# Optimization experiments

Measured on AMD Instinct MI355X. Metric: run time of the kernel, lower is better.

Reference implementation:

```python
import jax, jax.numpy as jnp
import numpy as np

CHUNK = 64  # mamba chunk size


def _ssd_chunk_scan(x, dt, A, Bs, Cs, R):
    """Exact chunked selective scan (mamba_chunk_scan_combined math, no D skip).
    x: [B,L,H,P] (H=K*R heads), dt: [B,L,H] (already softplus'd),
    A: [H], Bs/Cs: [B,L,K,N] groups (head h uses group h//R).
    Returns y: [B,L,H,P]."""
    Bsz, L, Hh, P = x.shape
    K, N = Bs.shape[2], Bs.shape[3]
    Nc = L // CHUNK
    # broadcast groups -> heads (head k*R+r uses group k)
    Bh = jnp.repeat(Bs, R, axis=2)  # [B,L,H,N]
    Ch = jnp.repeat(Cs, R, axis=2)
    xc = x.reshape(Bsz, Nc, CHUNK, Hh, P)
    dtc = dt.reshape(Bsz, Nc, CHUNK, Hh)
    Bc = Bh.reshape(Bsz, Nc, CHUNK, Hh, N)
    Cc = Ch.reshape(Bsz, Nc, CHUNK, Hh, N)
    dA = jnp.transpose(dtc, (0, 1, 3, 2)) * A[None, None, :, None]  # [B,Nc,H,Q]
    Acum = jnp.cumsum(dA, axis=-1)
    # intra-chunk decay matrix Lmat[i,j] = exp(sum_{j<s<=i} dA_s), lower-tri
    diff = Acum[..., :, None] - Acum[..., None, :]  # [B,Nc,H,Q,Q]
    tri = jnp.tril(jnp.ones((CHUNK, CHUNK), bool))
    Lmat = jnp.where(tri, jnp.exp(diff), 0.0)
    xdt = xc * dtc[..., None]  # dt enters as dt_j * B_j * x_j
    Y_diag = jnp.einsum('bcqhn,bcshn,bchqs,bcshp->bcqhp', Cc, Bc, Lmat, xdt)
    # chunk end states
    decay_last = jnp.exp(Acum[..., -1:] - Acum)  # [B,Nc,H,Q]
    states = jnp.einsum('bcqhn,bchq,bcqhp->bchpn', Bc, decay_last, xdt)
    chunk_decay = jnp.exp(Acum[..., -1])  # [B,Nc,H]
    def step(S, inp):
        cd, st = inp
        return cd[..., None, None] * S + st, S  # emit state BEFORE this chunk
    S0 = jnp.zeros((Bsz, Hh, P, N), x.dtype)
    _, prev = jax.lax.scan(step, S0, (jnp.moveaxis(chunk_decay, 1, 0), jnp.moveaxis(states, 1, 0)))
    prev = jnp.moveaxis(prev, 0, 1)  # [B,Nc,H,P,N]
    Y_off = jnp.einsum('bcqhn,bchpn,bchq->bcqhp', Cc, prev, jnp.exp(Acum))
    return (Y_diag + Y_off).reshape(Bsz, L, Hh, P)


def _forward(x, in_proj_w, conv_w, conv_b, x_proj_w, A_logs, Ds, dt_bias,
             out_norm_g, out_norm_b, out_proj_w):
    B, H, W, Dm = x.shape
    K, R = A_logs.shape
    P = Ds.shape[2]               # headdim
    d_inner = x_proj_w.shape[2]
    N = (x_proj_w.shape[1] - R) // 2
    L = H * W
    # in_proj + gate split
    xz = jnp.einsum('bhwc,dc->bhwd', x, in_proj_w)
    xi, z = jnp.split(xz, 2, axis=-1)
    z = jax.nn.gelu(z, approximate=False)
    # depthwise 3x3 conv (torch weight [d_inner,1,3,3] -> HWIO [3,3,1,d_inner])
    kern = jnp.transpose(conv_w, (2, 3, 1, 0))
    xi = jax.lax.conv_general_dilated(xi, kern, (1, 1), 'SAME',
            dimension_numbers=('NHWC', 'HWIO', 'NHWC'),
            feature_group_count=d_inner) + conv_b
    xi = jax.nn.gelu(xi, approximate=False)
    # cross2d scan: row-major, col-major, and their reverses
    x0 = xi.reshape(B, L, d_inner)
    x1 = jnp.transpose(xi, (0, 2, 1, 3)).reshape(B, L, d_inner)
    xs = jnp.stack([x0, x1, x0[:, ::-1], x1[:, ::-1]], axis=2)  # [B,L,K,d_inner]
    x_dbl = jnp.einsum('blkd,kcd->blkc', xs, x_proj_w)
    dts = x_dbl[..., :R].reshape(B, L, K * R)
    Bs = x_dbl[..., R:R + N]
    Cs = x_dbl[..., R + N:]
    xs_h = xs.reshape(B, L, K * R, P)
    A = -jnp.exp(A_logs.astype(jnp.float32)).reshape(K * R)
    Dmat = Ds.astype(jnp.float32).reshape(K * R, P)
    dt = jax.nn.softplus(dts + dt_bias.reshape(K * R))
    ys = _ssd_chunk_scan(xs_h, dt, A, Bs, Cs, R) + xs_h * Dmat  # D skip on raw x
    ys = ys.reshape(B, L, K, d_inner)
    # cross merge: invert each scan order, sum over K
    def unT(y):
        return jnp.transpose(y.reshape(B, W, H, d_inner), (0, 2, 1, 3)).reshape(B, L, d_inner)
    y = ys[:, :, 0] + ys[:, ::-1, 2] + unT(ys[:, :, 1]) + unT(ys[:, ::-1, 3])
    # out LayerNorm
    y = y.reshape(B, H, W, d_inner)
    mu = y.mean(-1, keepdims=True)
    var = y.var(-1, keepdims=True)
    y = (y - mu) / jnp.sqrt(var + 1e-5) * out_norm_g + out_norm_b
    y = y * z  # gating
    return jnp.einsum('bhwd,cd->bhwc', y, out_proj_w)


def setup_inputs() -> dict:
    key = jax.random.key(0)
    ks = jax.random.split(key, 10)
    B, H, W, Dm = 2, 64, 64, 192
    d_inner, K, R, N = 384, 4, 12, 64
    P = d_inner // R  # 32
    s = 0.02
    return {
        'x': jax.random.normal(ks[0], (B, H, W, Dm), jnp.float32),
        'in_proj_w': s * jax.random.normal(ks[1], (2 * d_inner, Dm), jnp.float32),
        'conv_w': s * jax.random.normal(ks[2], (d_inner, 1, 3, 3), jnp.float32),
        'conv_b': s * jax.random.normal(ks[3], (d_inner,), jnp.float32),
        'x_proj_w': s * jax.random.normal(ks[4], (K, R + 2 * N, d_inner), jnp.float32),
        'A_logs': 0.5 * jax.random.normal(ks[5], (K, R), jnp.float32),
        'Ds': jax.random.uniform(ks[6], (K, R, P), jnp.float32),
        'dt_bias': 0.1 * jax.random.uniform(ks[7], (K, R), jnp.float32),
        'out_norm_g': jnp.ones((d_inner,), jnp.float32),
        'out_norm_b': jnp.zeros((d_inner,), jnp.float32),
        'out_proj_w': s * jax.random.normal(ks[8], (Dm, d_inner), jnp.float32),
    }


def reference(x, in_proj_w, conv_w, conv_b, x_proj_w, A_logs, Ds, dt_bias,
              out_norm_g, out_norm_b, out_proj_w):
    return _forward(x, in_proj_w, conv_w, conv_b, x_proj_w, A_logs, Ds, dt_bias,
                    out_norm_g, out_norm_b, out_proj_w)
```

## Files before the change

### kernel.cpp

```cpp
#include <hip/hip_runtime.h>
#include <math.h>

#define DI 384

typedef __attribute__((ext_vector_type(8))) short bf8v;
typedef __attribute__((ext_vector_type(4))) float f4v;

__device__ __forceinline__ f4v mfma16(bf8v a, bf8v b, f4v c) {
  return __builtin_amdgcn_mfma_f32_16x16x32_bf16(a, b, c, 0, 0, 0);
}

__device__ __forceinline__ int trf(int l) { return ((l & 63) << 6) | (l >> 6); }
__device__ __forceinline__ int mapk(int k, int l) {
  if (k == 0) return l;
  if (k == 1) return trf(l);
  if (k == 2) return 4095 - l;
  return trf(4095 - l);
}
__device__ __forceinline__ float gelu_f(float x) {
  return 0.5f * x * (1.0f + erff(x * 0.7071067811865475f));
}
__device__ __forceinline__ float softplus_f(float x) {
  return (x > 20.0f) ? x : log1pf(expf(x));
}
__device__ __forceinline__ unsigned short f2bf(float f) {
  unsigned u = __float_as_uint(f);
  unsigned r = (u + 0x7fff + ((u >> 16) & 1)) >> 16;
  return (unsigned short)r;
}
__device__ __forceinline__ float bf2f(unsigned short h) {
  return __uint_as_float(((unsigned)h) << 16);
}
__device__ __forceinline__ unsigned short el16(uint2 v, int i) {
  unsigned w = (i < 2) ? v.x : v.y;
  return (unsigned short)((i & 1) ? (w >> 16) : (w & 0xffffu));
}
__device__ __forceinline__ void cvt8v(const float* __restrict__ p, bf8v& hv, bf8v& lv) {
#pragma unroll
  for (int i = 0; i < 8; ++i) {
    float v = p[i];
    unsigned short h = f2bf(v);
    hv[i] = (short)h;
    lv[i] = (short)f2bf(v - bf2f(h));
  }
}
__device__ __forceinline__ int swz(int row, int col) {
  return (row << 6) + ((((col >> 3) ^ (row & 7)) << 3) | (col & 7));
}
__device__ __forceinline__ int foff(int row, int cb) {
  return (row << 6) + ((cb ^ (row & 7)) << 3);
}

__global__ __launch_bounds__(256) void k_inproj(const float* __restrict__ x,
                                                const float* __restrict__ wip,
                                                unsigned short* __restrict__ xr_hi,
                                                unsigned short* __restrict__ xr_lo,
                                                float* __restrict__ zg) {
  const int K = 192;
  __shared__ unsigned short Ah[4096], Al[4096], Bh[4096], Bl[4096];
  int tid = threadIdx.x;
  int lane = tid & 63, w = tid >> 6;
  int cl = lane & 15, kb = lane >> 4;
  int wm = w >> 1, wn = w & 1;
  int m0 = blockIdx.y * 64, n0 = blockIdx.x * 64;
  f4v acc[2][2];
  acc[0][0] = acc[0][1] = acc[1][0] = acc[1][1] = (f4v){0.f, 0.f, 0.f, 0.f};
  for (int k0 = 0; k0 < K; k0 += 64) {
#pragma unroll
    for (int u = 0; u < 2; ++u) {
      int unit = tid + u * 256;
      int row = unit >> 3, blk = unit & 7;
      int e = foff(row, blk);
      bf8v hv, lv;
      cvt8v(x + (size_t)(m0 + row) * K + k0 + blk * 8, hv, lv);
      *(bf8v*)(Ah + e) = hv;
      *(bf8v*)(Al + e) = lv;
      cvt8v(wip + (size_t)(n0 + row) * K + k0 + blk * 8, hv, lv);
      *(bf8v*)(Bh + e) = hv;
      *(bf8v*)(Bl + e) = lv;
    }
    __syncthreads();
#pragma unroll
    for (int chunk = 0; chunk < 2; ++chunk) {
      int cb = chunk * 4 + kb;
      bf8v ah[2], al[2], bh[2], bl[2];
#pragma unroll
      for (int mi = 0; mi < 2; ++mi) {
        ah[mi] = *(const bf8v*)(Ah + foff(wm * 32 + mi * 16 + cl, cb));
        al[mi] = *(const bf8v*)(Al + foff(wm * 32 + mi * 16 + cl, cb));
      }
#pragma unroll
      for (int ni = 0; ni < 2; ++ni) {
        bh[ni] = *(const bf8v*)(Bh + foff(wn * 32 + ni * 16 + cl, cb));
        bl[ni] = *(const bf8v*)(Bl + foff(wn * 32 + ni * 16 + cl, cb));
      }
#pragma unroll
      for (int mi = 0; mi < 2; ++mi)
#pragma unroll
        for (int ni = 0; ni < 2; ++ni) {
          acc[mi][ni] = mfma16(ah[mi], bh[ni], acc[mi][ni]);
          acc[mi][ni] = mfma16(ah[mi], bl[ni], acc[mi][ni]);
          acc[mi][ni] = mfma16(al[mi], bh[ni], acc[mi][ni]);
        }
    }
    __syncthreads();
  }
#pragma unroll
  for (int mi = 0; mi < 2; ++mi)
#pragma unroll
    for (int ni = 0; ni < 2; ++ni)
#pragma unroll
      for (int i = 0; i < 4; ++i) {
        int m = m0 + wm * 32 + mi * 16 + kb * 4 + i;
        int n = n0 + wn * 32 + ni * 16 + cl;
        float v = acc[mi][ni][i];
        if (n < DI) {
          unsigned short hh = f2bf(v);
          xr_hi[(size_t)m * DI + n] = hh;
          xr_lo[(size_t)m * DI + n] = f2bf(v - bf2f(hh));
        } else {
          zg[(size_t)m * DI + (n - DI)] = gelu_f(v);
        }
      }
}

__global__ __launch_bounds__(256) void k_conv(const unsigned short* __restrict__ xrh,
                                              const unsigned short* __restrict__ xrl,
                                              const float* __restrict__ cw,
                                              const float* __restrict__ cb,
                                              unsigned short* __restrict__ xhi,
                                              unsigned short* __restrict__ xlo,
                                              unsigned short* __restrict__ xthi,
                                              unsigned short* __restrict__ xtlo) {
  int idx = blockIdx.x * 256 + threadIdx.x;
  int c = idx % DI;
  int lf = idx / DI;
  int b = lf >> 12;
  int l = lf & 4095;
  int h = l >> 6, w = l & 63;
  float acc = cb[c];
#pragma unroll
  for (int dh = -1; dh <= 1; ++dh) {
    int hh = h + dh;
    if ((unsigned)hh >= 64u) continue;
#pragma unroll
    for (int dw = -1; dw <= 1; ++dw) {
      int ww = w + dw;
      if ((unsigned)ww >= 64u) continue;
      size_t o = ((size_t)((b << 12) | (hh << 6) | ww)) * DI + c;
      acc += (bf2f(xrh[o]) + bf2f(xrl[o])) * cw[c * 9 + (dh + 1) * 3 + (dw + 1)];
    }
  }
  float g = gelu_f(acc);
  unsigned short hv = f2bf(g);
  unsigned short lv = f2bf(g - bf2f(hv));
  xhi[(size_t)idx] = hv;
  xlo[(size_t)idx] = lv;
  size_t tof = ((size_t)((b << 12) | trf(l))) * DI + c;
  xthi[tof] = hv;
  xtlo[tof] = lv;
}

__global__ __launch_bounds__(256) void k_xproj(const unsigned short* __restrict__ xhi,
                                               const unsigned short* __restrict__ xlo,
                                               const float* __restrict__ wxp,
                                               const float* __restrict__ dt_bias,
                                               float* __restrict__ dt_buf,
                                               unsigned short* __restrict__ Bhi,
                                               unsigned short* __restrict__ Blo,
                                               unsigned short* __restrict__ Chi,
                                               unsigned short* __restrict__ Clo) {
  const int K = DI, N = 140;
  int kdir = blockIdx.z;
  __shared__ unsigned short Ah[4096], Al[4096], Bh[4096], Bl[4096];
  __shared__ int rowbase[64];
  int tid = threadIdx.x;
  int lane = tid & 63, w = tid >> 6;
  int cl = lane & 15, kb = lane >> 4;
  int wm = w >> 1, wn = w & 1;
  int m0 = blockIdx.y * 64, n0 = blockIdx.x * 64;
  if (tid < 64) {
    int m = m0 + tid;
    int b = m >> 12, l = m & 4095;
    rowbase[tid] = (b << 12) + mapk(kdir, l);
  }
  const float* wk = wxp + (size_t)kdir * N * K;
  f4v acc[2][2];
  acc[0][0] = acc[0][1] = acc[1][0] = acc[1][1] = (f4v){0.f, 0.f, 0.f, 0.f};
  __syncthreads();
  for (int k0 = 0; k0 < K; k0 += 64) {
#pragma unroll
    for (int u = 0; u < 2; ++u) {
      int unit = tid + u * 256;
      int row = unit >> 3, blk = unit & 7;
      int e = foff(row, blk);
      size_t ga = (size_t)rowbase[row] * DI + k0 + blk * 8;
      *(bf8v*)(Ah + e) = *(const bf8v*)(xhi + ga);
      *(bf8v*)(Al + e) = *(const bf8v*)(xlo + ga);
      int n = n0 + row;
      if (n < N) {
        bf8v hv, lv;
        cvt8v(wk + (size_t)n * K + k0 + blk * 8, hv, lv);
        *(bf8v*)(Bh + e) = hv;
        *(bf8v*)(Bl + e) = lv;
      } else {
        bf8v z = {0, 0, 0, 0, 0, 0, 0, 0};
        *(bf8v*)(Bh + e) = z;
        *(bf8v*)(Bl + e) = z;
      }
    }
    __syncthreads();
#pragma unroll
    for (int chunk = 0; chunk < 2; ++chunk) {
      int cb = chunk * 4 + kb;
      bf8v ah[2], al[2], bh[2], bl[2];
#pragma unroll
      for (int mi = 0; mi < 2; ++mi) {
        ah[mi] = *(const bf8v*)(Ah + foff(wm * 32 + mi * 16 + cl, cb));
        al[mi] = *(const bf8v*)(Al + foff(wm * 32 + mi * 16 + cl, cb));
      }
#pragma unroll
      for (int ni = 0; ni < 2; ++ni) {
        bh[ni] = *(const bf8v*)(Bh + foff(wn * 32 + ni * 16 + cl, cb));
        bl[ni] = *(const bf8v*)(Bl + foff(wn * 32 + ni * 16 + cl, cb));
      }
#pragma unroll
      for (int mi = 0; mi < 2; ++mi)
#pragma unroll
        for (int ni = 0; ni < 2; ++ni) {
          acc[mi][ni] = mfma16(ah[mi], bh[ni], acc[mi][ni]);
          acc[mi][ni] = mfma16(ah[mi], bl[ni], acc[mi][ni]);
          acc[mi][ni] = mfma16(al[mi], bh[ni], acc[mi][ni]);
        }
    }
    __syncthreads();
  }
#pragma unroll
  for (int mi = 0; mi < 2; ++mi)
#pragma unroll
    for (int ni = 0; ni < 2; ++ni)
#pragma unroll
      for (int i = 0; i < 4; ++i) {
        int m = m0 + wm * 32 + mi * 16 + kb * 4 + i;
        int n = n0 + wn * 32 + ni * 16 + cl;
        if (n >= N) continue;
        float v = acc[mi][ni][i];
        int b = m >> 12, l = m & 4095;
        if (n < 12) {
          dt_buf[(((size_t)(b * 48 + kdir * 12 + n)) << 12) + l] =
              softplus_f(v + dt_bias[kdir * 12 + n]);
        } else if (n < 76) {
          size_t off = (((size_t)((b * 4 + kdir) << 12)) + l) * 64 + (n - 12);
          unsigned short hh = f2bf(v);
          Bhi[off] = hh;
          Blo[off] = f2bf(v - bf2f(hh));
        } else {
          size_t off = (((size_t)((b * 4 + kdir) << 12)) + l) * 64 + (n - 76);
          unsigned short hh = f2bf(v);
          Chi[off] = hh;
          Clo[off] = f2bf(v - bf2f(hh));
        }
      }
}

__global__ __launch_bounds__(256) void k_dtacum(const float* __restrict__ dt_buf,
                                                const float* __restrict__ A_logs,
                                                float* __restrict__ ac_buf,
                                                float* __restrict__ cdec) {
  int bh = blockIdx.y;
  int c = blockIdx.x * 4 + (threadIdx.x >> 6);
  int lane = threadIdx.x & 63;
  int h = bh % 48;
  size_t o = ((size_t)bh << 12) + c * 64 + lane;
  float dtv = dt_buf[o];
  float v = dtv * (-__expf(A_logs[h]));
#pragma unroll
  for (int off = 1; off < 64; off <<= 1) {
    float u = __shfl_up(v, off, 64);
    if (lane >= off) v += u;
  }
  ac_buf[o] = v;
  if (lane == 63) cdec[bh * 64 + c] = __expf(v);
}

__global__ __launch_bounds__(256) void k_states(const unsigned short* __restrict__ xhi,
                                                const unsigned short* __restrict__ xthi,
                                                const float* __restrict__ dt_buf,
                                                const float* __restrict__ ac_buf,
                                                const unsigned short* __restrict__ Bhi,
                                                unsigned short* __restrict__ Shi) {
  int c = blockIdx.x, k = blockIdx.y >> 1, g = blockIdx.y & 1, b = blockIdx.z;
  __shared__ unsigned short Bt_h[4096];
  __shared__ unsigned short xwb[2][2048];
  int tid = threadIdx.x;
  int lane = tid & 63, w = tid >> 6;
  int cl = lane & 15, kb = lane >> 4;
  const unsigned short* xp = (k & 1) ? xthi : xhi;
  int pg = tid & 7, qq = tid >> 3;
  int h0_ = k * 12 + g * 6;
  uint2 xgA[2], xgB[2];
#pragma unroll
  for (int qp = 0; qp < 2; ++qp) {
    int i = c * 64 + qq * 2 + qp;
    if (k & 2) i = 4095 - i;
    xgA[qp] = *(const uint2*)(xp + ((size_t)((b << 12) + i)) * DI + (g * 6) * 32 + pg * 4);
  }
  size_t dto0 = (((size_t)(b * 48 + h0_)) << 12) + c * 64 + lane;
  float dtA = dt_buf[dto0];
  float acA = ac_buf[dto0];
  float dtB, acB;
  size_t Bbase = (((size_t)((b * 4 + k) << 12)) + c * 64) * 64;
  {
    int n = lane;
#pragma unroll
    for (int it = 0; it < 8; ++it) {
      int q0 = 2 * (w + it * 4);
      unsigned short h0 = Bhi[Bbase + (size_t)q0 * 64 + n];
      unsigned short h1 = Bhi[Bbase + (size_t)(q0 + 1) * 64 + n];
      *(unsigned int*)(Bt_h + swz(n, q0)) = (unsigned)h0 | ((unsigned)h1 << 16);
    }
  }
  for (int rr = 0; rr < 6; ++rr) {
    int r = g * 6 + rr;
    int h = k * 12 + r;
    float v = acA;
    float alast = __shfl(v, 63, 64);
    float wq = dtA * __expf(alast - v);
    float w0 = __shfl(wq, qq * 2, 64), w1 = __shfl(wq, qq * 2 + 1, 64);
    unsigned short* xw_h = xwb[rr & 1];
#pragma unroll
    for (int pi = 0; pi < 4; ++pi) {
      int p = pg * 4 + pi;
      unsigned short h0 = f2bf(bf2f(el16(xgA[0], pi)) * w0);
      unsigned short h1 = f2bf(bf2f(el16(xgA[1], pi)) * w1);
      *(unsigned int*)(xw_h + swz(p, qq * 2)) = (unsigned)h0 | ((unsigned)h1 << 16);
    }
    __syncthreads();
    if (rr < 5) {
#pragma unroll
      for (int qp = 0; qp < 2; ++qp) {
        int i = c * 64 + qq * 2 + qp;
        if (k & 2) i = 4095 - i;
        xgB[qp] = *(const uint2*)(xp + ((size_t)((b << 12) + i)) * DI + (r + 1) * 32 + pg * 4);
      }
      size_t dton = (((size_t)(b * 48 + h + 1)) << 12) + c * 64 + lane;
      dtB = dt_buf[dton];
      acB = ac_buf[dton];
    }
    f4v acc0 = {0.f, 0.f, 0.f, 0.f}, acc1 = {0.f, 0.f, 0.f, 0.f};
#pragma unroll
    for (int chunk = 0; chunk < 2; ++chunk) {
      int cb_ = chunk * 4 + kb;
      bf8v bh = *(const bf8v*)(Bt_h + foff(w * 16 + cl, cb_));
      bf8v a0h = *(const bf8v*)(xw_h + foff(cl, cb_));
      bf8v a1h = *(const bf8v*)(xw_h + foff(16 + cl, cb_));
      acc0 = mfma16(a0h, bh, acc0);
      acc1 = mfma16(a1h, bh, acc1);
    }
    size_t sbase = ((size_t)(b * 48 + h) * 64 + c) * 2048;
#pragma unroll
    for (int i = 0; i < 4; ++i) {
      int prow = kb * 4 + i;
      int n = w * 16 + cl;
      Shi[sbase + (size_t)prow * 64 + n] = f2bf(acc0[i]);
      Shi[sbase + (size_t)(16 + prow) * 64 + n] = f2bf(acc1[i]);
    }
    xgA[0] = xgB[0];
    xgA[1] = xgB[1];
    dtA = dtB;
    acA = acB;
  }
}

__global__ __launch_bounds__(256) void k_scan(unsigned short* __restrict__ Shi,
                                              const float* __restrict__ cdec) {
  int j = blockIdx.x;
  int bh = blockIdx.y;
  int tid = threadIdx.x;
  size_t base0 = (size_t)bh * 64 * 2048 + j * 256 + tid;
  float S = 0.0f;
  float nxt = bf2f(Shi[base0]);
  for (int c = 0; c < 64; ++c) {
    float cd = cdec[bh * 64 + c];
    size_t idx = base0 + (size_t)c * 2048;
    float tmp = nxt;
    if (c < 63) nxt = bf2f(Shi[idx + 2048]);
    Shi[idx] = f2bf(S);
    S = cd * S + tmp;
  }
}

__global__ __launch_bounds__(256) void k_out(const unsigned short* __restrict__ xhi,
                                             const unsigned short* __restrict__ xlo,
                                             const unsigned short* __restrict__ xthi,
                                             const unsigned short* __restrict__ xtlo,
                                             const float* __restrict__ dt_buf,
                                             const float* __restrict__ ac_buf,
                                             const unsigned short* __restrict__ Bhi,
                                             const unsigned short* __restrict__ Blo,
                                             const unsigned short* __restrict__ Chi,
                                             const unsigned short* __restrict__ Clo,
                                             const float* __restrict__ Ds,
                                             const unsigned short* __restrict__ Phi,
                                             float* __restrict__ ys) {
  int c = blockIdx.x, k = blockIdx.y >> 1, g = blockIdx.y & 1, b = blockIdx.z;
  __shared__ unsigned short C_h[4096], C_l[4096];
  __shared__ unsigned short Gb[2][4096];
  __shared__ unsigned short Xb[2][4096];
  int tid = threadIdx.x;
  int lane = tid & 63, w = tid >> 6;
  int cl = lane & 15, kb = lane >> 4;
  const unsigned short* xph = (k & 1) ? xthi : xhi;
  const unsigned short* xpl = (k & 1) ? xtlo : xlo;
  int pg = tid & 7, sq = tid >> 3;
  int h0_ = k * 12 + g * 6;
  uint2 xghA[2], xglA[2], xghB[2], xglB[2];
#pragma unroll
  for (int sp = 0; sp < 2; ++sp) {
    int i = c * 64 + sq * 2 + sp;
    if (k & 2) i = 4095 - i;
    size_t o = ((size_t)((b << 12) + i)) * DI + (g * 6) * 32 + pg * 4;
    xghA[sp] = *(const uint2*)(xph + o);
    xglA[sp] = *(const uint2*)(xpl + o);
  }
  bf8v pfA[2][2], pfB[2][2];
  {
    size_t pb = ((size_t)(b * 48 + h0_) * 64 + c) * 2048;
#pragma unroll
    for (int chunk = 0; chunk < 2; ++chunk) {
      int cb_ = chunk * 4 + kb;
      pfA[chunk][0] = *(const bf8v*)(Phi + pb + (size_t)cl * 64 + cb_ * 8);
      pfA[chunk][1] = *(const bf8v*)(Phi + pb + (size_t)(16 + cl) * 64 + cb_ * 8);
    }
  }
  size_t dto0 = (((size_t)(b * 48 + h0_)) << 12) + c * 64 + lane;
  float dtA = dt_buf[dto0];
  float vA = ac_buf[dto0];
  float dtB, vB;
  size_t base64 = (((size_t)((b * 4 + k) << 12)) + c * 64) * 64;
  {
    int n0 = (tid & 31) * 2;
    int qq = tid >> 5;
#pragma unroll
    for (int it = 0; it < 8; ++it) {
      int q = qq + it * 8;
      size_t off = base64 + (size_t)q * 64 + n0;
      int e = swz(q, n0);
      *(unsigned int*)(C_h + e) = *(const unsigned int*)(Chi + off);
      *(unsigned int*)(C_l + e) = *(const unsigned int*)(Clo + off);
      *(unsigned int*)(Gb[0] + e) = *(const unsigned int*)(Bhi + off);
      *(unsigned int*)(Gb[1] + e) = *(const unsigned int*)(Blo + off);
    }
  }
  __syncthreads();
  bf8v caf_h[2], caf_l[2];
#pragma unroll
  for (int chunk = 0; chunk < 2; ++chunk) {
    caf_h[chunk] = *(const bf8v*)(C_h + foff(w * 16 + cl, chunk * 4 + kb));
    caf_l[chunk] = *(const bf8v*)(C_l + foff(w * 16 + cl, chunk * 4 + kb));
  }
  f4v cbt[4];
#pragma unroll
  for (int St = 0; St < 4; ++St) cbt[St] = (f4v){0.f, 0.f, 0.f, 0.f};
#pragma unroll
  for (int St = 0; St < 4; ++St) {
    int srow = St * 16 + cl;
#pragma unroll
    for (int chunk = 0; chunk < 2; ++chunk) {
      bf8v bh = *(const bf8v*)(Gb[0] + foff(srow, chunk * 4 + kb));
      bf8v bl = *(const bf8v*)(Gb[1] + foff(srow, chunk * 4 + kb));
      cbt[St] = mfma16(caf_h[chunk], bh, cbt[St]);
      cbt[St] = mfma16(caf_h[chunk], bl, cbt[St]);
      cbt[St] = mfma16(caf_l[chunk], bh, cbt[St]);
    }
  }
  __syncthreads();
  for (int rr = 0; rr < 6; ++rr) {
    int r = g * 6 + rr;
    int h = k * 12 + r;
    float dtv = dtA;
    float v = vA;
    float ea = __expf(v);
    unsigned short* Gc = Gb[rr & 1];
    unsigned short* X_h = Xb[rr & 1];
    unsigned short* X_l = Xb[rr & 1] + 2048;
#pragma unroll
    for (int pi = 0; pi < 4; ++pi) {
      int p = pg * 4 + pi;
      int e = swz(p, sq * 2);
      *(unsigned int*)(X_h + e) =
          (unsigned)el16(xghA[0], pi) | ((unsigned)el16(xghA[1], pi) << 16);
      *(unsigned int*)(X_l + e) =
          (unsigned)el16(xglA[0], pi) | ((unsigned)el16(xglA[1], pi) << 16);
    }
    float vq[4], evq[4];
#pragma unroll
    for (int i = 0; i < 4; ++i) {
      vq[i] = __shfl(v, w * 16 + kb * 4 + i, 64);
      evq[i] = __shfl(ea, w * 16 + kb * 4 + i, 64);
    }
#pragma unroll
    for (int St = 0; St < 4; ++St) {
      int s = St * 16 + cl;
      float vs = __shfl(v, s, 64);
      float dts = __shfl(dtv, s, 64);
#pragma unroll
      for (int i = 0; i < 4; ++i) {
        int q = w * 16 + kb * 4 + i;
        float gv = (q >= s) ? cbt[St][i] * __expf(vq[i] - vs) * dts : 0.0f;
        Gc[swz(q, s)] = f2bf(gv);
      }
    }
    __syncthreads();
    if (rr < 5) {
#pragma unroll
      for (int sp = 0; sp < 2; ++sp) {
        int i = c * 64 + sq * 2 + sp;
        if (k & 2) i = 4095 - i;
        size_t o = ((size_t)((b << 12) + i)) * DI + (r + 1) * 32 + pg * 4;
        xghB[sp] = *(const uint2*)(xph + o);
        xglB[sp] = *(const uint2*)(xpl + o);
      }
      size_t pbn = ((size_t)(b * 48 + h + 1) * 64 + c) * 2048;
#pragma unroll
      for (int chunk = 0; chunk < 2; ++chunk) {
        int cb_ = chunk * 4 + kb;
        pfB[chunk][0] = *(const bf8v*)(Phi + pbn + (size_t)cl * 64 + cb_ * 8);
        pfB[chunk][1] = *(const bf8v*)(Phi + pbn + (size_t)(16 + cl) * 64 + cb_ * 8);
      }
      size_t dton = (((size_t)(b * 48 + h + 1)) << 12) + c * 64 + lane;
      dtB = dt_buf[dton];
      vB = ac_buf[dton];
    }
    f4v aD0 = {0.f, 0.f, 0.f, 0.f}, aD1 = aD0, aO0 = aD0, aO1 = aD0;
#pragma unroll
    for (int chunk = 0; chunk < 2; ++chunk) {
      int cb_ = chunk * 4 + kb;
      int qrow = w * 16 + cl;
      bf8v gh = *(const bf8v*)(Gc + foff(qrow, cb_));
      bf8v x0h = *(const bf8v*)(X_h + foff(cl, cb_));
      bf8v x0l = *(const bf8v*)(X_l + foff(cl, cb_));
      bf8v x1h = *(const bf8v*)(X_h + foff(16 + cl, cb_));
      bf8v x1l = *(const bf8v*)(X_l + foff(16 + cl, cb_));
      aD0 = mfma16(gh, x0h, aD0);
      aD0 = mfma16(gh, x0l, aD0);
      aD1 = mfma16(gh, x1h, aD1);
      aD1 = mfma16(gh, x1l, aD1);
      aO0 = mfma16(caf_h[chunk], pfA[chunk][0], aO0);
      aO0 = mfma16(caf_l[chunk], pfA[chunk][0], aO0);
      aO1 = mfma16(caf_h[chunk], pfA[chunk][1], aO1);
      aO1 = mfma16(caf_l[chunk], pfA[chunk][1], aO1);
    }
    float D0 = Ds[h * 32 + cl], D1 = Ds[h * 32 + 16 + cl];
    size_t ybase = ((size_t)((b * 4 + k) << 12) + c * 64) * DI + r * 32;
#pragma unroll
    for (int i = 0; i < 4; ++i) {
      int q = w * 16 + kb * 4 + i;
      float eaq = evq[i];
      int e0 = swz(cl, q), e1 = swz(16 + cl, q);
      float xv0 = bf2f(X_h[e0]) + bf2f(X_l[e0]);
      float xv1 = bf2f(X_h[e1]) + bf2f(X_l[e1]);
      ys[ybase + (size_t)q * DI + cl] = aD0[i] + eaq * aO0[i] + D0 * xv0;
      ys[ybase + (size_t)q * DI + 16 + cl] = aD1[i] + eaq * aO1[i] + D1 * xv1;
    }
#pragma unroll
    for (int chunk = 0; chunk < 2; ++chunk) {
      pfA[chunk][0] = pfB[chunk][0];
      pfA[chunk][1] = pfB[chunk][1];
    }
    xghA[0] = xghB[0]; xghA[1] = xghB[1];
    xglA[0] = xglB[0]; xglA[1] = xglB[1];
    dtA = dtB;
    vA = vB;
  }
}

__global__ __launch_bounds__(128) void k_ln(const float* __restrict__ ys,
                                            const float* __restrict__ zg,
                                            const float* __restrict__ gg,
                                            const float* __restrict__ bb,
                                            unsigned short* __restrict__ y2h,
                                            unsigned short* __restrict__ y2l) {
  int row = blockIdx.x;
  int b = row >> 12, l = row & 4095;
  int l1 = trf(l);
  int l2 = 4095 - l;
  int l3 = 4095 - l1;
  int tid = threadIdx.x;
  float v[3];
  size_t base = ((size_t)(b * 4)) << 12;
#pragma unroll
  for (int j = 0; j < 3; ++j) {
    int d = tid + j * 128;
    v[j] = ys[(base + l) * DI + d] + ys[(base + 4096 + l1) * DI + d] +
           ys[(base + 8192 + l2) * DI + d] + ys[(base + 12288 + l3) * DI + d];
  }
  __shared__ float red[2];
  float s = v[0] + v[1] + v[2];
#pragma unroll
  for (int off = 32; off > 0; off >>= 1) s += __shfl_down(s, off, 64);
  if ((tid & 63) == 0) red[tid >> 6] = s;
  __syncthreads();
  float mu = (red[0] + red[1]) * (1.0f / 384.0f);
  __syncthreads();
  float d2 = 0.0f;
#pragma unroll
  for (int j = 0; j < 3; ++j) {
    float dd = v[j] - mu;
    d2 += dd * dd;
  }
#pragma unroll
  for (int off = 32; off > 0; off >>= 1) d2 += __shfl_down(d2, off, 64);
  if ((tid & 63) == 0) red[tid >> 6] = d2;
  __syncthreads();
  float rstd = rsqrtf((red[0] + red[1]) * (1.0f / 384.0f) + 1e-5f);
#pragma unroll
  for (int j = 0; j < 3; ++j) {
    int d = tid + j * 128;
    float yv = (v[j] - mu) * rstd * gg[d] + bb[d];
    float o = yv * zg[(size_t)row * DI + d];
    unsigned short hh = f2bf(o);
    y2h[(size_t)row * DI + d] = hh;
    y2l[(size_t)row * DI + d] = f2bf(o - bf2f(hh));
  }
}

__global__ __launch_bounds__(256) void k_outproj(const unsigned short* __restrict__ Ahi,
                                                 const unsigned short* __restrict__ Alo,
                                                 const float* __restrict__ wop,
                                                 float* __restrict__ out) {
  const int K = DI, NO = 192;
  __shared__ unsigned short Ah[4096], Al[4096], Bh[4096], Bl[4096];
  int tid = threadIdx.x;
  int lane = tid & 63, w = tid >> 6;
  int cl = lane & 15, kb = lane >> 4;
  int wm = w >> 1, wn = w & 1;
  int m0 = blockIdx.y * 64, n0 = blockIdx.x * 64;
  f4v acc[2][2];
  acc[0][0] = acc[0][1] = acc[1][0] = acc[1][1] = (f4v){0.f, 0.f, 0.f, 0.f};
  for (int k0 = 0; k0 < K; k0 += 64) {
#pragma unroll
    for (int u = 0; u < 2; ++u) {
      int unit = tid + u * 256;
      int row = unit >> 3, blk = unit & 7;
      int e = foff(row, blk);
      size_t ga = (size_t)(m0 + row) * K + k0 + blk * 8;
      *(bf8v*)(Ah + e) = *(const bf8v*)(Ahi + ga);
      *(bf8v*)(Al + e) = *(const bf8v*)(Alo + ga);
      bf8v hv, lv;
      cvt8v(wop + (size_t)(n0 + row) * K + k0 + blk * 8, hv, lv);
      *(bf8v*)(Bh + e) = hv;
      *(bf8v*)(Bl + e) = lv;
    }
    __syncthreads();
#pragma unroll
    for (int chunk = 0; chunk < 2; ++chunk) {
      int cb = chunk * 4 + kb;
      bf8v ah[2], al[2], bh[2], bl[2];
#pragma unroll
      for (int mi = 0; mi < 2; ++mi) {
        ah[mi] = *(const bf8v*)(Ah + foff(wm * 32 + mi * 16 + cl, cb));
        al[mi] = *(const bf8v*)(Al + foff(wm * 32 + mi * 16 + cl, cb));
      }
#pragma unroll
      for (int ni = 0; ni < 2; ++ni) {
        bh[ni] = *(const bf8v*)(Bh + foff(wn * 32 + ni * 16 + cl, cb));
        bl[ni] = *(const bf8v*)(Bl + foff(wn * 32 + ni * 16 + cl, cb));
      }
#pragma unroll
      for (int mi = 0; mi < 2; ++mi)
#pragma unroll
        for (int ni = 0; ni < 2; ++ni) {
          acc[mi][ni] = mfma16(ah[mi], bh[ni], acc[mi][ni]);
          acc[mi][ni] = mfma16(ah[mi], bl[ni], acc[mi][ni]);
          acc[mi][ni] = mfma16(al[mi], bh[ni], acc[mi][ni]);
        }
    }
    __syncthreads();
  }
#pragma unroll
  for (int mi = 0; mi < 2; ++mi)
#pragma unroll
    for (int ni = 0; ni < 2; ++ni)
#pragma unroll
      for (int i = 0; i < 4; ++i) {
        int m = m0 + wm * 32 + mi * 16 + kb * 4 + i;
        int n = n0 + wn * 32 + ni * 16 + cl;
        out[(size_t)m * NO + n] = acc[mi][ni][i];
      }
}

extern "C" void kernel_launch(void* const* d_in, const int* in_sizes, int n_in,
                              void* d_out, int out_size, void* d_ws, size_t ws_size,
                              hipStream_t stream) {
  const float* x = (const float*)d_in[0];
  const float* in_proj_w = (const float*)d_in[1];
  const float* conv_w = (const float*)d_in[2];
  const float* conv_b = (const float*)d_in[3];
  const float* x_proj_w = (const float*)d_in[4];
  const float* A_logs = (const float*)d_in[5];
  const float* Ds = (const float*)d_in[6];
  const float* dt_bias = (const float*)d_in[7];
  const float* out_norm_g = (const float*)d_in[8];
  const float* out_norm_b = (const float*)d_in[9];
  const float* out_proj_w = (const float*)d_in[10];
  float* out = (float*)d_out;

  float* ws = (float*)d_ws;
  float* xi_raw = ws;
  float* zg = xi_raw + 3145728;
  float* dt_buf = zg + 3145728;
  float* ac_buf = dt_buf + 393216;
  float* cdec = ac_buf + 393216;
  float* ys = cdec + 6144;
  unsigned short* u16p = (unsigned short*)(ys + 12582912);
  unsigned short* Shi = u16p;    u16p += 12582912;
  unsigned short* xi_hi = u16p;  u16p += 3145728;
  unsigned short* xi_lo = u16p;  u16p += 3145728;
  unsigned short* xit_hi = u16p; u16p += 3145728;
  unsigned short* xit_lo = u16p; u16p += 3145728;
  unsigned short* Bhi = u16p;    u16p += 2097152;
  unsigned short* Blo = u16p;    u16p += 2097152;
  unsigned short* Chi = u16p;    u16p += 2097152;
  unsigned short* Clo = u16p;    u16p += 2097152;
  unsigned short* xr_hi = (unsigned short*)xi_raw;
  unsigned short* xr_lo = xr_hi + 3145728;
  unsigned short* y2h = xr_hi;
  unsigned short* y2l = y2h + 3145728;

  k_inproj<<<dim3(12, 128), 256, 0, stream>>>(x, in_proj_w, xr_hi, xr_lo, zg);
  k_conv<<<dim3(12288), 256, 0, stream>>>(xr_hi, xr_lo, conv_w, conv_b, xi_hi, xi_lo,
                                          xit_hi, xit_lo);
  k_xproj<<<dim3(3, 128, 4), 256, 0, stream>>>(xi_hi, xi_lo, x_proj_w, dt_bias,
                                               dt_buf, Bhi, Blo, Chi, Clo);
  k_dtacum<<<dim3(16, 96), 256, 0, stream>>>(dt_buf, A_logs, ac_buf, cdec);
  k_states<<<dim3(64, 8, 2), 256, 0, stream>>>(xi_hi, xit_hi, dt_buf, ac_buf, Bhi, Shi);
  k_scan<<<dim3(8, 96), 256, 0, stream>>>(Shi, cdec);
  k_out<<<dim3(64, 8, 2), 256, 0, stream>>>(xi_hi, xi_lo, xit_hi, xit_lo, dt_buf,
                                            ac_buf, Bhi, Blo, Chi, Clo, Ds, Shi, ys);
  k_ln<<<dim3(8192), 128, 0, stream>>>(ys, zg, out_norm_g, out_norm_b, y2h, y2l);
  k_outproj<<<dim3(3, 128), 256, 0, stream>>>(y2h, y2l, out_proj_w, out);
}
```

Before: 179.1 us.

## Share x tile across forward and reversed scan directions in x_proj GEMM

The x_proj kernel now handles two scan directions per block: direction k and k+2 use the same spatial rows (forward vs reversed), so one A tile from either the row-major or transposed activation copy feeds both weight matrices. Reversal is applied at write-out by mirroring the sequence index, and the row-gather indirection is removed in favour of reading the pre-transposed copy. This halves activation tile loads and grid blocks, at the cost of more LDS and doubled accumulators per thread, which may lower occupancy.

```diff
diff --git a/kernel.cpp b/kernel.cpp
--- a/kernel.cpp
+++ b/kernel.cpp
@@ -11,12 +11,6 @@
 }
 
 __device__ __forceinline__ int trf(int l) { return ((l & 63) << 6) | (l >> 6); }
-__device__ __forceinline__ int mapk(int k, int l) {
-  if (k == 0) return l;
-  if (k == 1) return trf(l);
-  if (k == 2) return 4095 - l;
-  return trf(4095 - l);
-}
 __device__ __forceinline__ float gelu_f(float x) {
   return 0.5f * x * (1.0f + erff(x * 0.7071067811865475f));
 }
@@ -163,6 +157,8 @@
 
 __global__ __launch_bounds__(256) void k_xproj(const unsigned short* __restrict__ xhi,
                                                const unsigned short* __restrict__ xlo,
+                                               const unsigned short* __restrict__ xthi,
+                                               const unsigned short* __restrict__ xtlo,
                                                const float* __restrict__ wxp,
                                                const float* __restrict__ dt_bias,
                                                float* __restrict__ dt_buf,
@@ -171,49 +167,56 @@
                                                unsigned short* __restrict__ Chi,
                                                unsigned short* __restrict__ Clo) {
   const int K = DI, N = 140;
-  int kdir = blockIdx.z;
-  __shared__ unsigned short Ah[4096], Al[4096], Bh[4096], Bl[4096];
-  __shared__ int rowbase[64];
+  int z = blockIdx.z;
+  __shared__ unsigned short Ah[4096], Al[4096];
+  __shared__ unsigned short B0h[4096], B0l[4096], B1h[4096], B1l[4096];
   int tid = threadIdx.x;
   int lane = tid & 63, w = tid >> 6;
   int cl = lane & 15, kb = lane >> 4;
   int wm = w >> 1, wn = w & 1;
   int m0 = blockIdx.y * 64, n0 = blockIdx.x * 64;
-  if (tid < 64) {
-    int m = m0 + tid;
-    int b = m >> 12, l = m & 4095;
-    rowbase[tid] = (b << 12) + mapk(kdir, l);
-  }
-  const float* wk = wxp + (size_t)kdir * N * K;
-  f4v acc[2][2];
-  acc[0][0] = acc[0][1] = acc[1][0] = acc[1][1] = (f4v){0.f, 0.f, 0.f, 0.f};
-  __syncthreads();
+  const unsigned short* xph = z ? xthi : xhi;
+  const unsigned short* xpl = z ? xtlo : xlo;
+  const float* wk0 = wxp + (size_t)z * N * K;
+  const float* wk1 = wxp + (size_t)(z + 2) * N * K;
+  f4v acc[2][2][2];
+#pragma unroll
+  for (int d = 0; d < 2; ++d)
+#pragma unroll
+    for (int mi = 0; mi < 2; ++mi)
+#pragma unroll
+      for (int ni = 0; ni < 2; ++ni) acc[d][mi][ni] = (f4v){0.f, 0.f, 0.f, 0.f};
   for (int k0 = 0; k0 < K; k0 += 64) {
 #pragma unroll
     for (int u = 0; u < 2; ++u) {
       int unit = tid + u * 256;
       int row = unit >> 3, blk = unit & 7;
       int e = foff(row, blk);
-      size_t ga = (size_t)rowbase[row] * DI + k0 + blk * 8;
-      *(bf8v*)(Ah + e) = *(const bf8v*)(xhi + ga);
-      *(bf8v*)(Al + e) = *(const bf8v*)(xlo + ga);
+      size_t ga = (size_t)(m0 + row) * DI + k0 + blk * 8;
+      *(bf8v*)(Ah + e) = *(const bf8v*)(xph + ga);
+      *(bf8v*)(Al + e) = *(const bf8v*)(xpl + ga);
       int n = n0 + row;
       if (n < N) {
         bf8v hv, lv;
-        cvt8v(wk + (size_t)n * K + k0 + blk * 8, hv, lv);
-        *(bf8v*)(Bh + e) = hv;
-        *(bf8v*)(Bl + e) = lv;
+        cvt8v(wk0 + (size_t)n * K + k0 + blk * 8, hv, lv);
+        *(bf8v*)(B0h + e) = hv;
+        *(bf8v*)(B0l + e) = lv;
+        cvt8v(wk1 + (size_t)n * K + k0 + blk * 8, hv, lv);
+        *(bf8v*)(B1h + e) = hv;
+        *(bf8v*)(B1l + e) = lv;
       } else {
-        bf8v z = {0, 0, 0, 0, 0, 0, 0, 0};
-        *(bf8v*)(Bh + e) = z;
-        *(bf8v*)(Bl + e) = z;
+        bf8v zv = {0, 0, 0, 0, 0, 0, 0, 0};
+        *(bf8v*)(B0h + e) = zv;
+        *(bf8v*)(B0l + e) = zv;
+        *(bf8v*)(B1h + e) = zv;
+        *(bf8v*)(B1l + e) = zv;
       }
     }
     __syncthreads();
 #pragma unroll
     for (int chunk = 0; chunk < 2; ++chunk) {
       int cb = chunk * 4 + kb;
-      bf8v ah[2], al[2], bh[2], bl[2];
+      bf8v ah[2], al[2];
 #pragma unroll
       for (int mi = 0; mi < 2; ++mi) {
         ah[mi] = *(const bf8v*)(Ah + foff(wm * 32 + mi * 16 + cl, cb));
@@ -221,46 +224,56 @@
       }
 #pragma unroll
       for (int ni = 0; ni < 2; ++ni) {
-        bh[ni] = *(const bf8v*)(Bh + foff(wn * 32 + ni * 16 + cl, cb));
-        bl[ni] = *(const bf8v*)(Bl + foff(wn * 32 + ni * 16 + cl, cb));
-      }
-#pragma unroll
-      for (int mi = 0; mi < 2; ++mi)
-#pragma unroll
-        for (int ni = 0; ni < 2; ++ni) {
-          acc[mi][ni] = mfma16(ah[mi], bh[ni], acc[mi][ni]);
-          acc[mi][ni] = mfma16(ah[mi], bl[ni], acc[mi][ni]);
-          acc[mi][ni] = mfma16(al[mi], bh[ni], acc[mi][ni]);
+        int brow = wn * 32 + ni * 16 + cl;
+        bf8v b0h = *(const bf8v*)(B0h + foff(brow, cb));
+        bf8v b0l = *(const bf8v*)(B0l + foff(brow, cb));
+        bf8v b1h = *(const bf8v*)(B1h + foff(brow, cb));
+        bf8v b1l = *(const bf8v*)(B1l + foff(brow, cb));
+#pragma unroll
+        for (int mi = 0; mi < 2; ++mi) {
+          acc[0][mi][ni] = mfma16(ah[mi], b0h, acc[0][mi][ni]);
+          acc[0][mi][ni] = mfma16(ah[mi], b0l, acc[0][mi][ni]);
+          acc[0][mi][ni] = mfma16(al[mi], b0h, acc[0][mi][ni]);
+          acc[1][mi][ni] = mfma16(ah[mi], b1h, acc[1][mi][ni]);
+          acc[1][mi][ni] = mfma16(ah[mi], b1l, acc[1][mi][ni]);
+          acc[1][mi][ni] = mfma16(al[mi], b1h, acc[1][mi][ni]);
         }
+      }
     }
     __syncthreads();
   }
 #pragma unroll
-  for (int mi = 0; mi < 2; ++mi)
-#pragma unroll
-    for (int ni = 0; ni < 2; ++ni)
-#pragma unroll
-      for (int i = 0; i < 4; ++i) {
-        int m = m0 + wm * 32 + mi * 16 + kb * 4 + i;
-        int n = n0 + wn * 32 + ni * 16 + cl;
-        if (n >= N) continue;
-        float v = acc[mi][ni][i];
-        int b = m >> 12, l = m & 4095;
-        if (n < 12) {
-          dt_buf[(((size_t)(b * 48 + kdir * 12 + n)) << 12) + l] =
-              softplus_f(v + dt_bias[kdir * 12 + n]);
-        } else if (n < 76) {
-          size_t off = (((size_t)((b * 4 + kdir) << 12)) + l) * 64 + (n - 12);
-          unsigned short hh = f2bf(v);
-          Bhi[off] = hh;
-          Blo[off] = f2bf(v - bf2f(hh));
-        } else {
-          size_t off = (((size_t)((b * 4 + kdir) << 12)) + l) * 64 + (n - 76);
-          unsigned short hh = f2bf(v);
-          Chi[off] = hh;
-          Clo[off] = f2bf(v - bf2f(hh));
+  for (int d = 0; d < 2; ++d) {
+    int kd = z + d * 2;
+#pragma unroll
+    for (int mi = 0; mi < 2; ++mi)
+#pragma unroll
+      for (int ni = 0; ni < 2; ++ni)
+#pragma unroll
+        for (int i = 0; i < 4; ++i) {
+          int m = m0 + wm * 32 + mi * 16 + kb * 4 + i;
+          int n = n0 + wn * 32 + ni * 16 + cl;
+          if (n >= N) continue;
+          float v = acc[d][mi][ni][i];
+          int b = m >> 12;
+          int l = m & 4095;
+          if (d) l = 4095 - l;
+          if (n < 12) {
+            dt_buf[(((size_t)(b * 48 + kd * 12 + n)) << 12) + l] =
+                softplus_f(v + dt_bias[kd * 12 + n]);
+          } else if (n < 76) {
+            size_t off = (((size_t)((b * 4 + kd) << 12)) + l) * 64 + (n - 12);
+            unsigned short hh = f2bf(v);
+            Bhi[off] = hh;
+            Blo[off] = f2bf(v - bf2f(hh));
+          } else {
+            size_t off = (((size_t)((b * 4 + kd) << 12)) + l) * 64 + (n - 76);
+            unsigned short hh = f2bf(v);
+            Chi[off] = hh;
+            Clo[off] = f2bf(v - bf2f(hh));
+          }
         }
-      }
+  }
 }
 
 __global__ __launch_bounds__(256) void k_dtacum(const float* __restrict__ dt_buf,
@@ -731,8 +744,8 @@
   k_inproj<<<dim3(12, 128), 256, 0, stream>>>(x, in_proj_w, xr_hi, xr_lo, zg);
   k_conv<<<dim3(12288), 256, 0, stream>>>(xr_hi, xr_lo, conv_w, conv_b, xi_hi, xi_lo,
                                           xit_hi, xit_lo);
-  k_xproj<<<dim3(3, 128, 4), 256, 0, stream>>>(xi_hi, xi_lo, x_proj_w, dt_bias,
-                                               dt_buf, Bhi, Blo, Chi, Clo);
+  k_xproj<<<dim3(3, 128, 2), 256, 0, stream>>>(xi_hi, xi_lo, xit_hi, xit_lo, x_proj_w,
+                                               dt_bias, dt_buf, Bhi, Blo, Chi, Clo);
   k_dtacum<<<dim3(16, 96), 256, 0, stream>>>(dt_buf, A_logs, ac_buf, cdec);
   k_states<<<dim3(64, 8, 2), 256, 0, stream>>>(xi_hi, xit_hi, dt_buf, ac_buf, Bhi, Shi);
   k_scan<<<dim3(8, 96), 256, 0, stream>>>(Shi, cdec);
```

Result: no change. 175.6 us (-1.9%).
